# Performance work log

Measured on AMD Instinct MI355X. Metric: run time of the kernel, lower is better.

Reference implementation:

```python
import jax, jax.numpy as jnp
import numpy as np

IN, H, F2, OUT, B = 257, 400, 600, 257, 16384


def setup_inputs() -> dict:
    key = jax.random.key(0)
    ks = jax.random.split(key, 32)
    n = lambda i, shape, s: jax.random.normal(ks[i], shape, jnp.float32) * s
    d = {
        "x": n(0, (IN, B), 1.0),
        "h1": n(1, (H, B), 1.0),
        "h2": n(2, (H, B), 1.0),
        # fc1: 257 -> 400
        "W_fc1": n(3, (H, IN), 0.05),
        "b_fc1": n(4, (H,), 0.05),
        # GRU layer 1 (hidden 400)
        "Wiz1": n(5, (H, H), 0.05), "Wir1": n(6, (H, H), 0.05), "Win1": n(7, (H, H), 0.05),
        "Whz1": n(8, (H, H), 0.05), "Whr1": n(9, (H, H), 0.05), "Whn1": n(10, (H, H), 0.05),
        "biz1": n(11, (H,), 0.05), "bir1": n(12, (H,), 0.05), "bin1": n(13, (H,), 0.05),
        "bhz1": n(14, (H,), 0.05), "bhr1": n(15, (H,), 0.05), "bhn1": n(16, (H,), 0.05),
        # GRU layer 2
        "Wiz2": n(17, (H, H), 0.05), "Wir2": n(18, (H, H), 0.05), "Win2": n(19, (H, H), 0.05),
        "Whz2": n(20, (H, H), 0.05), "Whr2": n(21, (H, H), 0.05), "Whn2": n(22, (H, H), 0.05),
        "biz2": n(23, (H,), 0.05), "bir2": n(24, (H,), 0.05), "bin2": n(25, (H,), 0.05),
        "bhz2": n(26, (H,), 0.05), "bhr2": n(27, (H,), 0.05), "bhn2": n(28, (H,), 0.05),
        # fc2: 400 -> 600, fc3: 600 -> 600, fc4: 600 -> 257
        "W_fc2": n(29, (F2, H), 0.05), "b_fc2": n(30, (F2,), 0.05),
        "W_fc3": n(31, (F2, F2), 0.05), "b_fc3": jnp.zeros((F2,), jnp.float32),
        "W_fc4": jax.random.normal(jax.random.fold_in(key, 100), (OUT, F2), jnp.float32) * 0.05,
        "b_fc4": jnp.zeros((OUT,), jnp.float32),
    }
    return d


def _gru_cell(xin, h, Wiz, Wir, Win, Whz, Whr, Whn, biz, bir, bin_, bhz, bhr, bhn):
    # xin: [H, B], h: [H, B]; column-vector convention W @ x, matching the source.
    r = jax.nn.sigmoid(Wir @ xin + bir[:, None] + Whr @ h + bhr[:, None])
    z = jax.nn.sigmoid(Wiz @ xin + biz[:, None] + Whz @ h + bhz[:, None])
    n_ = jnp.tanh(Win @ xin + bin_[:, None] + r * (Whn @ h + bhn[:, None]))
    return (1.0 - z) * n_ + z * h


def reference(x, h1, h2, W_fc1, b_fc1,
              Wiz1, Wir1, Win1, Whz1, Whr1, Whn1,
              biz1, bir1, bin1, bhz1, bhr1, bhn1,
              Wiz2, Wir2, Win2, Whz2, Whr2, Whn2,
              biz2, bir2, bin2, bhz2, bhr2, bhn2,
              W_fc2, b_fc2, W_fc3, b_fc3, W_fc4, b_fc4):
    fc1 = W_fc1 @ x + b_fc1[:, None]                       # [400, B]
    h1n = _gru_cell(fc1, h1, Wiz1, Wir1, Win1, Whz1, Whr1, Whn1,
                    biz1, bir1, bin1, bhz1, bhr1, bhn1)    # [400, B]
    h2n = _gru_cell(h1n, h2, Wiz2, Wir2, Win2, Whz2, Whr2, Whn2,
                    biz2, bir2, bin2, bhz2, bhr2, bhn2)    # [400, B]
    y = jax.nn.relu(W_fc2 @ h2n + b_fc2[:, None])          # [600, B]
    y = jax.nn.relu(W_fc3 @ y + b_fc3[:, None])            # [600, B]
    return jax.nn.sigmoid(W_fc4 @ y + b_fc4[:, None])      # [257, B]
```

## Files before the change

kernel.cpp:

```cpp
#include <hip/hip_runtime.h>
#include <math.h>


#define B_TOTAL 16384
#define H16_TOTAL 3452928L
#define PREP_TOTAL 3460352L

typedef _Float16 h8 __attribute__((ext_vector_type(8)));
typedef float f4 __attribute__((ext_vector_type(4)));

#define GLL(g, l) __builtin_amdgcn_global_load_lds(                         \
    (const __attribute__((address_space(1))) void*)(g),                     \
    (__attribute__((address_space(3))) void*)(l), 16, 0, 0)

#define MFMA(d, a_, b_) d = __builtin_amdgcn_mfma_f32_16x16x32_f16(a_, b_, d, 0, 0, 0)
#define WAITV5() asm volatile("s_waitcnt vmcnt(5)" ::: "memory")
#define WAITV0() asm volatile("s_waitcnt vmcnt(0)" ::: "memory")
#define WAITL0() asm volatile("s_waitcnt lgkmcnt(0)" ::: "memory")
#define BAR()    __builtin_amdgcn_s_barrier()

__device__ inline int swzg(int row, int c) { return row * 8 + (c ^ (row & 7)); }

__device__ inline void swz_bt_mt(int bid, int& bt, int& mt) {
  const int xcd = bid & 7;
  const int i = bid >> 3;
  bt = xcd * 16 + (i & 15);
  mt = i >> 4;
}
__device__ inline void swz64(int bid, int& bt, int& mt) {
  const int xcd = bid & 7;
  const int i = bid >> 3;
  bt = xcd * 8 + (i & 7);
  mt = i >> 3;
}

__constant__ int kJsrc[32] = {3, 5,6,7, 8,9,10, 17,18,19, 20,21,22, 29, 31, 33,
                              4, 11,12,13, 14,15,16, 23,24,25, 26,27,28, 30, 32, 34};
__constant__ int kJM[32]   = {400, 400,400,400, 400,400,400, 400,400,400, 400,400,400, 600, 600, 257,
                              400, 400,400,400, 400,400,400, 400,400,400, 400,400,400, 600, 600, 257};
__constant__ int kJK[32]   = {257, 400,400,400, 400,400,400, 400,400,400, 400,400,400, 400, 600, 600,
                              1,1,1,1, 1,1,1, 1,1,1, 1,1,1, 1, 1, 1};
__constant__ int kJKp[32]  = {320, 448,448,448, 448,448,448, 448,448,448, 448,448,448, 448, 640, 640,
                              1,1,1,1, 1,1,1, 1,1,1, 1,1,1, 1, 1, 1};
__constant__ long kJcum[33] = {0,143360,344064,544768,745472,946176,1146880,1347584,1548288,1748992,
  1949696,2150400,2351104,2551808,2838528,3248128,3452928,3453376,3453824,3454272,3454720,3455168,
  3455616,3456064,3456512,3456960,3457408,3457856,3458304,3458752,3459392,3460032,3460352};

struct SrcPtrs { const float* p[35]; };

__global__ __launch_bounds__(256) void prep_weights(SrcPtrs sp, _Float16* __restrict__ w16,
                                                    float* __restrict__ b32) {
  long w = (long)blockIdx.x * 256 + threadIdx.x;
  if (w >= PREP_TOTAL) return;
  int j = 0;
  #pragma unroll 1
  while (j < 31 && kJcum[j + 1] <= w) j++;
  long local = w - kJcum[j];
  int Kp = kJKp[j];
  int m = (int)(local / Kp);
  int k = (int)(local - (long)m * Kp);
  float v = 0.f;
  if (m < kJM[j] && k < kJK[j]) v = sp.p[kJsrc[j]][(long)m * kJK[j] + k];
  if (j < 16) w16[w] = (_Float16)v;
  else        b32[w - H16_TOTAL] = v;
}

__global__ __launch_bounds__(256) void transpose_in(const float* __restrict__ x,
                                                    const float* __restrict__ h1,
                                                    const float* __restrict__ h2,
                                                    _Float16* __restrict__ dx,
                                                    _Float16* __restrict__ dh1,
                                                    _Float16* __restrict__ dh2) {
  __shared__ float t[32][33];
  int b = blockIdx.x;
  const float* src; _Float16* dst; int F, nFT;
  if (b < 5120)        { src = x;  dst = dx;  F = 257; nFT = 10; }
  else if (b < 12288)  { b -= 5120;  src = h1; dst = dh1; F = 400; nFT = 14; }
  else                 { b -= 12288; src = h2; dst = dh2; F = 400; nFT = 14; }
  const int Fp = nFT * 32;
  const int ft = b % nFT;
  const int bt = b / nFT;
  const int ci = threadIdx.x & 31, ri = threadIdx.x >> 5;
  #pragma unroll
  for (int p = 0; p < 4; ++p) {
    int f = ft * 32 + ri + p * 8;
    float v = (f < F) ? src[(long)f * B_TOTAL + bt * 32 + ci] : 0.f;
    t[ri + p * 8][ci] = v;
  }
  __syncthreads();
  #pragma unroll
  for (int p = 0; p < 4; ++p) {
    int bb = bt * 32 + ri + p * 8;
    dst[(long)bb * Fp + ft * 32 + ci] = (_Float16)t[ci][ri + p * 8];
  }
}

__global__ __launch_bounds__(256) void transpose_out(const float* __restrict__ src,
                                                     float* __restrict__ dst) {
  __shared__ float t[32][33];
  const int nFT = 10;
  const int ft = blockIdx.x % nFT;
  const int bt = blockIdx.x / nFT;
  const int ci = threadIdx.x & 31, ri = threadIdx.x >> 5;
  #pragma unroll
  for (int p = 0; p < 4; ++p)
    t[ri + p * 8][ci] = src[(long)(bt * 32 + ri + p * 8) * 320 + ft * 32 + ci];
  __syncthreads();
  #pragma unroll
  for (int p = 0; p < 4; ++p) {
    int f = ft * 32 + ri + p * 8;
    if (f < 257) dst[(long)f * B_TOTAL + bt * 32 + ci] = t[ci][ri + p * 8];
  }
}

template <int ACT, int OUTF32, int K, int M>
__global__ __launch_bounds__(512, 4) void gemm_tn(const _Float16* __restrict__ A,
                                                  const _Float16* __restrict__ W,
                                                  const float* __restrict__ bias,
                                                  void* __restrict__ C) {
  constexpr int KT = K / 64;
  __shared__ __align__(16) _Float16 As2[2][256 * 64];
  __shared__ __align__(16) _Float16 Ws2[2][64 * 64];
  const int tid = threadIdx.x;
  const int l = tid & 63;
  const int w = tid >> 6;
  int bt, mt;
  swz64(blockIdx.x, bt, mt);
  const int wr = w >> 1, wc = w & 1;
  const int sc = ((l & 7) ^ (l >> 3)) * 8;
  const int srow = tid >> 3;

  const _Float16* ag = A + (long)(bt * 256 + srow) * K + sc;
  const _Float16* wg = W + (long)(mt * 64 + srow) * K + sc;

  f4 acc[4][2];
  #pragma unroll
  for (int i = 0; i < 4; ++i)
    #pragma unroll
    for (int jj = 0; jj < 2; ++jj) acc[i][jj] = (f4){0.f, 0.f, 0.f, 0.f};

  const int lg = l >> 4;
  const int arow = wr * 64 + (l & 15);
  const int wrow = wc * 32 + (l & 15);

  auto stage = [&](int b, int t) {
    #pragma unroll
    for (int j = 0; j < 4; ++j)
      GLL(ag + t * 64 + (long)j * 64 * K, (char*)As2[b] + j * 8192 + w * 1024);
    GLL(wg + t * 64, (char*)Ws2[b] + w * 1024);
  };

  stage(0, 0);
  WAITV0();
  BAR();
  #pragma unroll
  for (int i = 0; i < KT; ++i) {
    if (i + 1 < KT) { stage((i + 1) & 1, i + 1); WAITV5(); }
    else            { WAITV0(); }
    BAR();
    const h8* AsV = (const h8*)As2[i & 1];
    const h8* WsV = (const h8*)Ws2[i & 1];
    h8 b00 = WsV[swzg(wrow, lg)],      b01 = WsV[swzg(wrow, 4 | lg)];
    h8 b10 = WsV[swzg(wrow + 16, lg)], b11 = WsV[swzg(wrow + 16, 4 | lg)];
    #pragma unroll
    for (int fm = 0; fm < 4; ++fm) {
      h8 a0 = AsV[swzg(arow + fm * 16, lg)];
      h8 a1 = AsV[swzg(arow + fm * 16, 4 | lg)];
      MFMA(acc[fm][0], a0, b00); MFMA(acc[fm][0], a1, b01);
      MFMA(acc[fm][1], a0, b10); MFMA(acc[fm][1], a1, b11);
    }
    WAITL0();
    BAR();
  }

  const int jloc = wc * 32 + (l & 15);
  const int colBase = mt * 64 + jloc;
  if (OUTF32) {
    const int rowBase = bt * 256 + wr * 64 + (l >> 4) * 4;
    #pragma unroll
    for (int fn = 0; fn < 2; ++fn) {
      const float bb = bias[colBase + fn * 16];
      #pragma unroll
      for (int fm = 0; fm < 4; ++fm)
        #pragma unroll
        for (int r = 0; r < 4; ++r) {
          float x = acc[fm][fn][r] + bb;
          if (ACT == 2) x = 1.f / (1.f + __expf(-x));
          ((float*)C)[(long)(rowBase + fm * 16 + r) * M + colBase + fn * 16] = x;
        }
    }
  } else {
    _Float16* scr = (_Float16*)As2;
    const int rowLoc = wr * 64 + (l >> 4) * 4;
    #pragma unroll
    for (int fn = 0; fn < 2; ++fn) {
      const float bb = bias[colBase + fn * 16];
      #pragma unroll
      for (int fm = 0; fm < 4; ++fm)
        #pragma unroll
        for (int r = 0; r < 4; ++r) {
          float x = acc[fm][fn][r] + bb;
          if (ACT == 1) x = fmaxf(x, 0.f);
          scr[(rowLoc + fm * 16 + r) * 80 + jloc + fn * 16] = (_Float16)x;
        }
    }
    __syncthreads();
    const int rq = tid & 3;
    #pragma unroll
    for (int p = 0; p < 2; ++p) {
      const int rrow = p * 128 + (tid >> 2);
      h8 v0 = *(const h8*)(scr + rrow * 80 + rq * 16);
      h8 v1 = *(const h8*)(scr + rrow * 80 + rq * 16 + 8);
      _Float16* gp = (_Float16*)C + (long)(bt * 256 + rrow) * M + mt * 64 + rq * 16;
      *(h8*)gp = v0;
      *(h8*)(gp + 8) = v1;
    }
  }
}

__global__ __launch_bounds__(512, 4) void gemm_gru(const _Float16* __restrict__ Ax,
                                                   const _Float16* __restrict__ Ah,
                                                   const _Float16* __restrict__ Wi_,
                                                   const _Float16* __restrict__ Wh_,
                                                   const float* __restrict__ bi,
                                                   const float* __restrict__ bh,
                                                   _Float16* __restrict__ Hn) {
  __shared__ __align__(16) _Float16 As2[2][128 * 64];
  __shared__ __align__(16) _Float16 Ws2[2][3][64 * 64];
  const int tid = threadIdx.x;
  const int l = tid & 63;
  const int w = tid >> 6;
  int bt, mt;
  swz_bt_mt(blockIdx.x, bt, mt);
  const int wr = w >> 1, wc = w & 1;
  const int sc = ((l & 7) ^ (l >> 3)) * 8;
  const int srow = tid >> 3;

  const long arowg = (long)(bt * 128 + srow) * 448 + sc;
  const long wrowg = (long)(mt * 64 + srow) * 448 + sc;

  f4 acc[4][2][2];
  #pragma unroll
  for (int g = 0; g < 4; ++g)
    #pragma unroll
    for (int i = 0; i < 2; ++i)
      #pragma unroll
      for (int jj = 0; jj < 2; ++jj) acc[g][i][jj] = (f4){0.f, 0.f, 0.f, 0.f};

  const int lg = l >> 4;
  const int arow = wr * 32 + (l & 15);
  const int wrow = wc * 32 + (l & 15);

  auto stage = [&](int b, int i) {
    const _Float16* ab = (i >= 7) ? Ah : Ax;
    const _Float16* wb = (i >= 7) ? Wh_ : Wi_;
    const int kc = ((i >= 7) ? (mt + i - 6) % 7 : i) * 64;
    GLL(ab + arowg + kc, (char*)As2[b] + w * 1024);
    GLL(ab + arowg + kc + 64 * 448, (char*)As2[b] + w * 1024 + 8192);
    #pragma unroll
    for (int g = 0; g < 3; ++g)
      GLL(wb + wrowg + (long)g * 200704 + kc, (char*)Ws2[b][g] + w * 1024);
  };

  stage(0, 0);
  WAITV0();
  BAR();
  #pragma unroll
  for (int i = 0; i < 14; ++i) {
    if (i < 13) { stage((i + 1) & 1, i + 1); WAITV5(); }
    else        { WAITV0(); }
    BAR();
    const h8* AsV = (const h8*)As2[i & 1];
    const h8* WsV = (const h8*)Ws2[i & 1][0];
    h8 a00 = AsV[swzg(arow, lg)],      a01 = AsV[swzg(arow, 4 | lg)];
    h8 a10 = AsV[swzg(arow + 16, lg)], a11 = AsV[swzg(arow + 16, 4 | lg)];
    #pragma unroll
    for (int g = 0; g < 3; ++g) {
      const int d = (g == 2) ? ((i < 7) ? 2 : 3) : g;
      h8 b00 = WsV[g * 512 + swzg(wrow, lg)];
      h8 b01 = WsV[g * 512 + swzg(wrow, 4 | lg)];
      h8 b10 = WsV[g * 512 + swzg(wrow + 16, lg)];
      h8 b11 = WsV[g * 512 + swzg(wrow + 16, 4 | lg)];
      MFMA(acc[d][0][0], a00, b00); MFMA(acc[d][0][0], a01, b01);
      MFMA(acc[d][0][1], a00, b10); MFMA(acc[d][0][1], a01, b11);
      MFMA(acc[d][1][0], a10, b00); MFMA(acc[d][1][0], a11, b01);
      MFMA(acc[d][1][1], a10, b10); MFMA(acc[d][1][1], a11, b11);
    }
    WAITL0();
    BAR();
  }

  const _Float16* Alast = As2[1];
  _Float16* scr = (_Float16*)Ws2;
  const int jloc = wc * 32 + (l & 15);
  const int rowLoc = wr * 32 + (l >> 4) * 4;
  #pragma unroll
  for (int fn = 0; fn < 2; ++fn) {
    const int j = mt * 64 + jloc + fn * 16;
    const float bz = bi[j] + bh[j];
    const float br = bi[448 + j] + bh[448 + j];
    const float bnx = bi[896 + j], bnh = bh[896 + j];
    #pragma unroll
    for (int fm = 0; fm < 2; ++fm) {
      #pragma unroll
      for (int r = 0; r < 4; ++r) {
        const float zz = 1.f / (1.f + __expf(-(acc[0][fm][fn][r] + bz)));
        const float rr = 1.f / (1.f + __expf(-(acc[1][fm][fn][r] + br)));
        const float nn = (acc[2][fm][fn][r] + bnx) + rr * (acc[3][fm][fn][r] + bnh);
        const float th = 1.f - 2.f / (__expf(2.f * nn) + 1.f);
        const int row = rowLoc + fm * 16 + r;
        const int col = jloc + fn * 16;
        const float ho = (float)Alast[swzg(row, col >> 3) * 8 + (col & 7)];
        scr[row * 80 + col] = (_Float16)((1.f - zz) * th + zz * ho);
      }
    }
  }
  __syncthreads();
  const int rrow = tid >> 2, rq = tid & 3;
  h8 v0 = *(const h8*)(scr + rrow * 80 + rq * 16);
  h8 v1 = *(const h8*)(scr + rrow * 80 + rq * 16 + 8);
  _Float16* gp = Hn + (long)(bt * 128 + rrow) * 448 + mt * 64 + rq * 16;
  *(h8*)gp = v0;
  *(h8*)(gp + 8) = v1;
}

extern "C" void kernel_launch(void* const* d_in, const int* in_sizes, int n_in,
                              void* d_out, int out_size, void* d_ws, size_t ws_size,
                              hipStream_t stream) {
  char* ws = (char*)d_ws;
  _Float16* W16  = (_Float16*)(ws);
  float*    BIAS = (float*)(ws + 6905856L);
  _Float16* buf2 = (_Float16*)(ws + 6935552L);
  _Float16* buf3 = (_Float16*)(ws + 27907072L);
  _Float16* buf4 = (_Float16*)(ws + 48878592L);
  _Float16* buf5 = (_Float16*)(ws + 63558656L);
  _Float16* buf6 = (_Float16*)(ws + 78238720L);
  float* outT = (float*)buf2;
  if (ws_size < 92918784UL) return;

  SrcPtrs sp;
  for (int i = 0; i < 35; ++i) sp.p[i] = (const float*)d_in[i];

  prep_weights<<<dim3(13517), dim3(256), 0, stream>>>(sp, W16, BIAS);
  transpose_in<<<dim3(19456), dim3(256), 0, stream>>>((const float*)d_in[0], (const float*)d_in[1],
                                                      (const float*)d_in[2], buf2, buf4, buf5);

  gemm_tn<0, 0, 320, 448><<<dim3(64 * 7), dim3(512), 0, stream>>>(buf2, W16, BIAS, (void*)buf3);
  gemm_gru<<<dim3(128 * 7), dim3(512), 0, stream>>>(buf3, buf4, W16 + 143360, W16 + 745472,
                                                    BIAS + 448, BIAS + 1792, buf6);
  gemm_gru<<<dim3(128 * 7), dim3(512), 0, stream>>>(buf6, buf5, W16 + 1347584, W16 + 1949696,
                                                    BIAS + 3136, BIAS + 4480, buf4);
  gemm_tn<1, 0, 448, 640><<<dim3(64 * 10), dim3(512), 0, stream>>>(buf4, W16 + 2551808, BIAS + 5824, (void*)buf2);
  gemm_tn<1, 0, 640, 640><<<dim3(64 * 10), dim3(512), 0, stream>>>(buf2, W16 + 2838528, BIAS + 6464, (void*)buf3);
  gemm_tn<2, 1, 640, 320><<<dim3(64 * 5), dim3(512), 0, stream>>>(buf3, W16 + 3248128, BIAS + 7104, (void*)outT);

  transpose_out<<<dim3(10 * 512), dim3(256), 0, stream>>>(outT, (float*)d_out);
}
```

Before: 403.4 us.

## Merge prep and input transpose kernels, fuse output transpose into last GEMM

Merges the weight-conversion and input-transpose kernels into a single setup launch. The output transpose kernel is removed: the final GEMM epilogue applies the sigmoid and writes float4 vectors directly into the feature-major output, skipping padded columns. It also raises wave priority around the MFMA blocks with s_setprio and repacks the workspace buffers into a smaller footprint. This saves two launches and one full fp32 pass over the output, but the direct writes are strided by column, which may coalesce less well than the old transpose.

```diff
diff --git a/kernel.cpp b/kernel.cpp
--- a/kernel.cpp
+++ b/kernel.cpp
@@ -48,35 +48,34 @@
 
 struct SrcPtrs { const float* p[35]; };
 
-__global__ __launch_bounds__(256) void prep_weights(SrcPtrs sp, _Float16* __restrict__ w16,
-                                                    float* __restrict__ b32) {
-  long w = (long)blockIdx.x * 256 + threadIdx.x;
-  if (w >= PREP_TOTAL) return;
-  int j = 0;
-  #pragma unroll 1
-  while (j < 31 && kJcum[j + 1] <= w) j++;
-  long local = w - kJcum[j];
-  int Kp = kJKp[j];
-  int m = (int)(local / Kp);
-  int k = (int)(local - (long)m * Kp);
-  float v = 0.f;
-  if (m < kJM[j] && k < kJK[j]) v = sp.p[kJsrc[j]][(long)m * kJK[j] + k];
-  if (j < 16) w16[w] = (_Float16)v;
-  else        b32[w - H16_TOTAL] = v;
-}
-
-__global__ __launch_bounds__(256) void transpose_in(const float* __restrict__ x,
-                                                    const float* __restrict__ h1,
-                                                    const float* __restrict__ h2,
-                                                    _Float16* __restrict__ dx,
-                                                    _Float16* __restrict__ dh1,
-                                                    _Float16* __restrict__ dh2) {
+__global__ __launch_bounds__(256) void setup(SrcPtrs sp, _Float16* __restrict__ w16,
+                                             float* __restrict__ b32,
+                                             _Float16* __restrict__ dx,
+                                             _Float16* __restrict__ dh1,
+                                             _Float16* __restrict__ dh2) {
   __shared__ float t[32][33];
   int b = blockIdx.x;
+  if (b < 13517) {
+    long w = (long)b * 256 + threadIdx.x;
+    if (w >= PREP_TOTAL) return;
+    int j = 0;
+    #pragma unroll 1
+    while (j < 31 && kJcum[j + 1] <= w) j++;
+    long local = w - kJcum[j];
+    int Kp = kJKp[j];
+    int m = (int)(local / Kp);
+    int k = (int)(local - (long)m * Kp);
+    float v = 0.f;
+    if (m < kJM[j] && k < kJK[j]) v = sp.p[kJsrc[j]][(long)m * kJK[j] + k];
+    if (j < 16) w16[w] = (_Float16)v;
+    else        b32[w - H16_TOTAL] = v;
+    return;
+  }
+  b -= 13517;
   const float* src; _Float16* dst; int F, nFT;
-  if (b < 5120)        { src = x;  dst = dx;  F = 257; nFT = 10; }
-  else if (b < 12288)  { b -= 5120;  src = h1; dst = dh1; F = 400; nFT = 14; }
-  else                 { b -= 12288; src = h2; dst = dh2; F = 400; nFT = 14; }
+  if (b < 5120)        { src = sp.p[0]; dst = dx;  F = 257; nFT = 10; }
+  else if (b < 12288)  { b -= 5120;  src = sp.p[1]; dst = dh1; F = 400; nFT = 14; }
+  else                 { b -= 12288; src = sp.p[2]; dst = dh2; F = 400; nFT = 14; }
   const int Fp = nFT * 32;
   const int ft = b % nFT;
   const int bt = b / nFT;
@@ -95,25 +94,7 @@
   }
 }
 
-__global__ __launch_bounds__(256) void transpose_out(const float* __restrict__ src,
-                                                     float* __restrict__ dst) {
-  __shared__ float t[32][33];
-  const int nFT = 10;
-  const int ft = blockIdx.x % nFT;
-  const int bt = blockIdx.x / nFT;
-  const int ci = threadIdx.x & 31, ri = threadIdx.x >> 5;
-  #pragma unroll
-  for (int p = 0; p < 4; ++p)
-    t[ri + p * 8][ci] = src[(long)(bt * 32 + ri + p * 8) * 320 + ft * 32 + ci];
-  __syncthreads();
-  #pragma unroll
-  for (int p = 0; p < 4; ++p) {
-    int f = ft * 32 + ri + p * 8;
-    if (f < 257) dst[(long)f * B_TOTAL + bt * 32 + ci] = t[ci][ri + p * 8];
-  }
-}
-
-template <int ACT, int OUTF32, int K, int M>
+template <int ACT, int MODE, int K, int M>
 __global__ __launch_bounds__(512, 4) void gemm_tn(const _Float16* __restrict__ A,
                                                   const _Float16* __restrict__ W,
                                                   const float* __restrict__ bias,
@@ -162,6 +143,7 @@
     const h8* WsV = (const h8*)Ws2[i & 1];
     h8 b00 = WsV[swzg(wrow, lg)],      b01 = WsV[swzg(wrow, 4 | lg)];
     h8 b10 = WsV[swzg(wrow + 16, lg)], b11 = WsV[swzg(wrow + 16, 4 | lg)];
+    __builtin_amdgcn_s_setprio(1);
     #pragma unroll
     for (int fm = 0; fm < 4; ++fm) {
       h8 a0 = AsV[swzg(arow + fm * 16, lg)];
@@ -169,25 +151,29 @@
       MFMA(acc[fm][0], a0, b00); MFMA(acc[fm][0], a1, b01);
       MFMA(acc[fm][1], a0, b10); MFMA(acc[fm][1], a1, b11);
     }
+    __builtin_amdgcn_s_setprio(0);
     WAITL0();
     BAR();
   }
 
   const int jloc = wc * 32 + (l & 15);
   const int colBase = mt * 64 + jloc;
-  if (OUTF32) {
+  if (MODE == 2) {
     const int rowBase = bt * 256 + wr * 64 + (l >> 4) * 4;
     #pragma unroll
     for (int fn = 0; fn < 2; ++fn) {
-      const float bb = bias[colBase + fn * 16];
-      #pragma unroll
-      for (int fm = 0; fm < 4; ++fm)
+      const int col = colBase + fn * 16;
+      if (col < 257) {
+        const float bb = bias[col];
         #pragma unroll
-        for (int r = 0; r < 4; ++r) {
-          float x = acc[fm][fn][r] + bb;
-          if (ACT == 2) x = 1.f / (1.f + __expf(-x));
-          ((float*)C)[(long)(rowBase + fm * 16 + r) * M + colBase + fn * 16] = x;
+        for (int fm = 0; fm < 4; ++fm) {
+          f4 xv;
+          #pragma unroll
+          for (int r = 0; r < 4; ++r)
+            xv[r] = 1.f / (1.f + __expf(-(acc[fm][fn][r] + bb)));
+          *(f4*)((float*)C + (long)col * B_TOTAL + rowBase + fm * 16) = xv;
         }
+      }
     }
   } else {
     _Float16* scr = (_Float16*)As2;
@@ -274,6 +260,7 @@
     const h8* WsV = (const h8*)Ws2[i & 1][0];
     h8 a00 = AsV[swzg(arow, lg)],      a01 = AsV[swzg(arow, 4 | lg)];
     h8 a10 = AsV[swzg(arow + 16, lg)], a11 = AsV[swzg(arow + 16, 4 | lg)];
+    __builtin_amdgcn_s_setprio(1);
     #pragma unroll
     for (int g = 0; g < 3; ++g) {
       const int d = (g == 2) ? ((i < 7) ? 2 : 3) : g;
@@ -286,6 +273,7 @@
       MFMA(acc[d][1][0], a10, b00); MFMA(acc[d][1][0], a11, b01);
       MFMA(acc[d][1][1], a10, b10); MFMA(acc[d][1][1], a11, b11);
     }
+    __builtin_amdgcn_s_setprio(0);
     WAITL0();
     BAR();
   }
@@ -328,31 +316,29 @@
                               void* d_out, int out_size, void* d_ws, size_t ws_size,
                               hipStream_t stream) {
   char* ws = (char*)d_ws;
-  _Float16* W16  = (_Float16*)(ws);
-  float*    BIAS = (float*)(ws + 6905856L);
-  _Float16* buf2 = (_Float16*)(ws + 6935552L);
-  _Float16* buf3 = (_Float16*)(ws + 27907072L);
-  _Float16* buf4 = (_Float16*)(ws + 48878592L);
-  _Float16* buf5 = (_Float16*)(ws + 63558656L);
-  _Float16* buf6 = (_Float16*)(ws + 78238720L);
-  float* outT = (float*)buf2;
-  if (ws_size < 92918784UL) return;
+  _Float16* W16   = (_Float16*)(ws);
+  float*    BIAS  = (float*)(ws + 6905856L);
+  _Float16* xT    = (_Float16*)(ws + 6935552L);
+  _Float16* fc1o  = (_Float16*)(ws + 17421312L);
+  _Float16* h1old = (_Float16*)(ws + 32101376L);
+  _Float16* h2old = (_Float16*)(ws + 46781440L);
+  _Float16* h1new = (_Float16*)(ws + 61461504L);
+  _Float16* y1    = xT;
+  _Float16* y2    = h2old;
+  _Float16* h2new = h1old;
+  if (ws_size < 76141568UL) return;
 
   SrcPtrs sp;
   for (int i = 0; i < 35; ++i) sp.p[i] = (const float*)d_in[i];
 
-  prep_weights<<<dim3(13517), dim3(256), 0, stream>>>(sp, W16, BIAS);
-  transpose_in<<<dim3(19456), dim3(256), 0, stream>>>((const float*)d_in[0], (const float*)d_in[1],
-                                                      (const float*)d_in[2], buf2, buf4, buf5);
-
-  gemm_tn<0, 0, 320, 448><<<dim3(64 * 7), dim3(512), 0, stream>>>(buf2, W16, BIAS, (void*)buf3);
-  gemm_gru<<<dim3(128 * 7), dim3(512), 0, stream>>>(buf3, buf4, W16 + 143360, W16 + 745472,
-                                                    BIAS + 448, BIAS + 1792, buf6);
-  gemm_gru<<<dim3(128 * 7), dim3(512), 0, stream>>>(buf6, buf5, W16 + 1347584, W16 + 1949696,
-                                                    BIAS + 3136, BIAS + 4480, buf4);
-  gemm_tn<1, 0, 448, 640><<<dim3(64 * 10), dim3(512), 0, stream>>>(buf4, W16 + 2551808, BIAS + 5824, (void*)buf2);
-  gemm_tn<1, 0, 640, 640><<<dim3(64 * 10), dim3(512), 0, stream>>>(buf2, W16 + 2838528, BIAS + 6464, (void*)buf3);
-  gemm_tn<2, 1, 640, 320><<<dim3(64 * 5), dim3(512), 0, stream>>>(buf3, W16 + 3248128, BIAS + 7104, (void*)outT);
-
-  transpose_out<<<dim3(10 * 512), dim3(256), 0, stream>>>(outT, (float*)d_out);
-}
+  setup<<<dim3(32973), dim3(256), 0, stream>>>(sp, W16, BIAS, xT, h1old, h2old);
+
+  gemm_tn<0, 0, 320, 448><<<dim3(64 * 7), dim3(512), 0, stream>>>(xT, W16, BIAS, (void*)fc1o);
+  gemm_gru<<<dim3(128 * 7), dim3(512), 0, stream>>>(fc1o, h1old, W16 + 143360, W16 + 745472,
+                                                    BIAS + 448, BIAS + 1792, h1new);
+  gemm_gru<<<dim3(128 * 7), dim3(512), 0, stream>>>(h1new, h2old, W16 + 1347584, W16 + 1949696,
+                                                    BIAS + 3136, BIAS + 4480, h2new);
+  gemm_tn<1, 0, 448, 640><<<dim3(64 * 10), dim3(512), 0, stream>>>(h2new, W16 + 2551808, BIAS + 5824, (void*)y1);
+  gemm_tn<1, 0, 640, 640><<<dim3(64 * 10), dim3(512), 0, stream>>>(y1, W16 + 2838528, BIAS + 6464, (void*)y2);
+  gemm_tn<2, 2, 640, 320><<<dim3(64 * 5), dim3(512), 0, stream>>>(y2, W16 + 3248128, BIAS + 7104, d_out);
+}
```

New measurement: 373.7 us. -7.4%, faster.
